# Kernel optimization log

Measured on AMD Instinct MI355X. Metric: run time of the kernel, lower is better.

Reference implementation:

```python
import jax, jax.numpy as jnp
import numpy as np

N_QUBITS = 4
N_LAYERS = 2


def setup_inputs() -> dict:
    key = jax.random.key(0)
    ks = jax.random.split(key, 8)
    B, S, D, H, O = 64, 4096, 20, 64, 3
    rn = lambda k, shape: jax.random.normal(k, shape, dtype=jnp.float32)
    sc = lambda fan: np.float32(1.0 / np.sqrt(fan))
    return {
        "x": rn(ks[0], (B, S, D)),
        "W_embed": rn(ks[1], (H, D)) * sc(D),
        "b_embed": jnp.zeros((H,), jnp.float32),
        "W_c2q": rn(ks[2], (N_QUBITS, H)) * sc(H),
        "b_c2q": jnp.zeros((N_QUBITS,), jnp.float32),
        "q_weights": rn(ks[3], (N_LAYERS, N_QUBITS, 3)) * np.float32(0.1),
        "W_q2c": rn(ks[4], (H, N_QUBITS)) * sc(N_QUBITS),
        "b_q2c": jnp.zeros((H,), jnp.float32),
        "W_out": rn(ks[5], (O, H)) * sc(H),
        "b_out": jnp.zeros((O,), jnp.float32),
    }


def _rot_matrix(phi, theta, omega):
    # PennyLane Rot(phi, theta, omega) = RZ(omega) @ RY(theta) @ RZ(phi)
    c = jnp.cos(theta * 0.5)
    s = jnp.sin(theta * 0.5)
    ep = jnp.exp(-0.5j * (phi + omega))  # e^{-i(phi+omega)/2}
    em = jnp.exp(-0.5j * (phi - omega))  # e^{-i(phi-omega)/2}
    row0 = jnp.stack([ep * c, -jnp.conj(em) * s])
    row1 = jnp.stack([em * s, jnp.conj(ep) * c])
    return jnp.stack([row0, row1]).astype(jnp.complex64)  # [2,2]


def _apply_1q(state, U, q):
    # state: [N,2,2,2,2], U: [2,2] shared across the batch
    ax = 1 + q
    s = jnp.moveaxis(state, ax, -1)
    s = jnp.einsum('...a,ba->...b', s, U)
    return jnp.moveaxis(s, -1, ax)


def _cnot(state, q):
    # control qubit q (axis 1+q), target qubit q+1 (axis 2+q)
    ac = 1 + q
    s0 = jnp.take(state, 0, axis=ac)
    # after removing control axis, the target axis index becomes ac
    s1 = jnp.flip(jnp.take(state, 1, axis=ac), axis=ac)
    return jnp.stack([s0, s1], axis=ac)


def _quantum_layer(q_in, weights):
    # q_in: [N, n_qubits] angles; weights: [n_layers, n_qubits, 3]
    half = q_in * 0.5
    v = jnp.stack([jnp.cos(half), jnp.sin(half)], axis=-1).astype(jnp.complex64)  # [N,4,2]
    # RY(inputs[i]) applied to |0...0> -> product state
    state = jnp.einsum('na,nb,nc,nd->nabcd', v[:, 0], v[:, 1], v[:, 2], v[:, 3])
    for layer in range(N_LAYERS):
        for q in range(N_QUBITS):
            U = _rot_matrix(weights[layer, q, 0], weights[layer, q, 1], weights[layer, q, 2])
            state = _apply_1q(state, U, q)
        for q in range(N_QUBITS - 1):
            state = _cnot(state, q)
    probs = state.real ** 2 + state.imag ** 2  # [N,2,2,2,2]
    z = []
    for q in range(N_QUBITS):
        axes = tuple(a for a in range(1, N_QUBITS + 1) if a != 1 + q)
        p = jnp.sum(probs, axis=axes)  # [N,2]
        z.append(p[:, 0] - p[:, 1])   # <Z_q>
    return jnp.stack(z, axis=-1)  # [N, n_qubits]


def reference(x, W_embed, b_embed, W_c2q, b_c2q, q_weights, W_q2c, b_q2c, W_out, b_out):
    B, S, _ = x.shape
    h = jax.nn.relu(jnp.einsum('bsd,hd->bsh', x, W_embed) + b_embed)      # [B,S,H]
    q_in = jnp.tanh(jnp.einsum('bsh,qh->bsq', h, W_c2q) + b_c2q)          # [B,S,4]
    z = _quantum_layer(q_in.reshape(B * S, N_QUBITS), q_weights)          # [B*S,4]
    z = z.reshape(B, S, N_QUBITS)
    h2 = jnp.einsum('bsq,hq->bsh', z, W_q2c) + b_q2c                      # [B,S,H]
    coords = jnp.einsum('bsh,oh->bso', h2, W_out) + b_out                 # [B,S,3]
    return coords
```

## Files before the change

kernel.cpp:

```cpp
#include <hip/hip_runtime.h>

typedef __bf16 bf16x8 __attribute__((ext_vector_type(8)));
typedef float f32x4 __attribute__((ext_vector_type(4)));
typedef float f32x2 __attribute__((ext_vector_type(2)));

#define NQ 4
#define NLAYERS 2

#define OFF_UCOEF 0
#define OFF_WC    64
#define OFF_UR    96
#define OFF_UI    352
#define OFF_W     608
#define OFF_G     704

__device__ __forceinline__ float fast_tanh(float v) {
  const float e = __expf(2.f * v);
  return 1.f - 2.f * __builtin_amdgcn_rcpf(e + 1.f);
}

__global__ __launch_bounds__(256, 4) void fused_kernel(
    const float* __restrict__ x,
    const float* __restrict__ Wemb,
    const float* __restrict__ bemb,
    const float* __restrict__ Wc2q,
    const float* __restrict__ bc2q,
    const float* __restrict__ qw,
    const float* __restrict__ Wq2c,
    const float* __restrict__ bq2c,
    const float* __restrict__ Wout,
    const float* __restrict__ bout,
    float* __restrict__ out, int N) {
  __shared__ __attribute__((aligned(16))) float smem[4 * 2048];
  __shared__ __attribute__((aligned(16))) float Cs01[3 * 56];
  __shared__ __attribute__((aligned(16))) float Cs2[3 * 28];
  __shared__ float offsS[3];

  if ((int)(blockIdx.x << 8) >= N) return;

  const int tid = threadIdx.x;
  const int lane = tid & 63;
  const int warp = tid >> 6;
  const int wbase = (int)(blockIdx.x << 8) + (warp << 6);
  const int g = lane >> 4;
  const int cc = lane & 15;
  float* ws = &smem[warp * 2048];
  const f32x4 zero4 = {0.f, 0.f, 0.f, 0.f};

  float4 xr[5];
  {
    const float4* x4 = reinterpret_cast<const float4*>(x);
    const size_t max4 = (size_t)N * 5 - 1;
    const size_t base4 = (size_t)wbase * 5;
#pragma unroll
    for (int i = 0; i < 5; ++i) {
      size_t gi = base4 + (size_t)(i * 64 + lane);
      xr[i] = x4[gi <= max4 ? gi : max4];
    }
  }

  bf16x8 Aemb[4];
#pragma unroll
  for (int ht = 0; ht < 4; ++ht) {
    const int h = ht * 16 + cc;
    const float* wr = Wemb + h * 20;
    float t0 = 0.f, t1 = 0.f, t2 = 0.f, t3 = 0.f, t4 = 0.f, t5 = 0.f, t6 = 0.f, t7 = 0.f;
    if (g < 2) {
      const float4 v0 = *(const float4*)(wr + g * 8);
      const float4 v1 = *(const float4*)(wr + g * 8 + 4);
      t0 = v0.x; t1 = v0.y; t2 = v0.z; t3 = v0.w;
      t4 = v1.x; t5 = v1.y; t6 = v1.z; t7 = v1.w;
    } else if (g == 2) {
      const float4 v0 = *(const float4*)(wr + 16);
      t0 = v0.x; t1 = v0.y; t2 = v0.z; t3 = v0.w;
      t4 = bemb[h];
    }
    Aemb[ht][0] = (__bf16)t0; Aemb[ht][1] = (__bf16)t1;
    Aemb[ht][2] = (__bf16)t2; Aemb[ht][3] = (__bf16)t3;
    Aemb[ht][4] = (__bf16)t4; Aemb[ht][5] = (__bf16)t5;
    Aemb[ht][6] = (__bf16)t6; Aemb[ht][7] = (__bf16)t7;
  }

  bf16x8 A2[2];
#pragma unroll
  for (int t = 0; t < 2; ++t) {
#pragma unroll
    for (int j = 0; j < 8; ++j) {
      const int mu = t * 32 + ((j >> 2) << 4) + (g << 2) + (j & 3);
      A2[t][j] = (__bf16)Wc2q[(cc & 3) * 64 + mu];
    }
  }

  if (tid < 64) {
    const int gate = tid >> 3, comp = tid & 7;
    const float phi   = qw[gate * 3 + 0];
    const float theta = qw[gate * 3 + 1];
    const float omega = qw[gate * 3 + 2];
    const bool mid = (comp >= 2 && comp <= 5);
    const float cs = mid ? __sinf(0.5f * theta) : __cosf(0.5f * theta);
    const float ang = mid ? -0.5f * (phi - omega) : -0.5f * (phi + omega);
    const float tr = ((comp & 1) == 0) ? __cosf(ang) : __sinf(ang);
    const float sgn = (comp == 2 || comp == 7) ? -1.f : 1.f;
    smem[OFF_UCOEF + gate * 8 + comp] = sgn * tr * cs;
  } else if (tid < 76) {
    const int e = tid - 64, o = e >> 2, q = e & 3;
    float s = 0.f;
    for (int h = 0; h < 64; ++h) s += Wout[o * 64 + h] * Wq2c[h * 4 + q];
    smem[OFF_WC + e] = s;
  } else if (tid < 79) {
    const int o = tid - 76;
    float s = bout[o];
    for (int h = 0; h < 64; ++h) s += Wout[o * 64 + h] * bq2c[h];
    offsS[o] = s;
  }
  __syncthreads();

  {
    const int col = tid >> 4, amp = tid & 15;
    float re = (amp == col) ? 1.f : 0.f, im = 0.f;
#pragma unroll
    for (int layer = 0; layer < NLAYERS; ++layer) {
#pragma unroll
      for (int q = 0; q < NQ; ++q) {
        const int gate = layer * NQ + q;
        const int bit = 8 >> q;
        const bool lo = !(amp & bit);
        const float cr1 = smem[OFF_UCOEF + gate * 8 + (lo ? 0 : 6)];
        const float ci1 = smem[OFF_UCOEF + gate * 8 + (lo ? 1 : 7)];
        const float cr2 = smem[OFF_UCOEF + gate * 8 + (lo ? 2 : 4)];
        const float ci2 = smem[OFF_UCOEF + gate * 8 + (lo ? 3 : 5)];
        const float pr = __shfl_xor(re, bit);
        const float pi = __shfl_xor(im, bit);
        const float mr = re, mi = im;
        re = cr1 * mr - ci1 * mi + cr2 * pr - ci2 * pi;
        im = cr1 * mi + ci1 * mr + cr2 * pi + ci2 * pr;
      }
#pragma unroll
      for (int q = 0; q < NQ - 1; ++q) {
        const int cb = 8 >> q, tb = 4 >> q;
        const float pr = __shfl_xor(re, tb);
        const float pi = __shfl_xor(im, tb);
        if (amp & cb) { re = pr; im = pi; }
      }
    }
    smem[OFF_UR + amp * 16 + col] = re;
    smem[OFF_UI + amp * 16 + col] = im;
  }
  if (tid < 48) {
    const int o = tid >> 4, k = tid & 15;
    float s = 0.f;
#pragma unroll
    for (int q = 0; q < NQ; ++q) {
      const float t = smem[OFF_WC + o * 4 + q];
      s += ((k >> (3 - q)) & 1) ? -t : t;
    }
    smem[OFF_W + tid] = s;
  }
  __syncthreads();

  {
    const int i = tid >> 4, j = tid & 15;
    float s0 = 0.f, s1 = 0.f, s2 = 0.f;
#pragma unroll
    for (int k = 0; k < 16; ++k) {
      const float S = smem[OFF_UR + k * 16 + i] * smem[OFF_UR + k * 16 + j] +
                      smem[OFF_UI + k * 16 + i] * smem[OFF_UI + k * 16 + j];
      s0 = fmaf(smem[OFF_W + k], S, s0);
      s1 = fmaf(smem[OFF_W + 16 + k], S, s1);
      s2 = fmaf(smem[OFF_W + 32 + k], S, s2);
    }
    smem[OFF_G + (i * 16 + j)] = s0;
    smem[OFF_G + 256 + (i * 16 + j)] = s1;
    smem[OFF_G + 512 + (i * 16 + j)] = s2;
  }
  __syncthreads();

  if (tid < 243) {
    const int o = tid / 81, t = tid % 81;
    const int tv0 = t / 27, tv1 = (t / 9) % 3, tv2 = (t / 3) % 3, tv3 = t % 3;
    const int tv[4] = {tv0, tv1, tv2, tv3};
    int xmask = 0, zmask = 0;
#pragma unroll
    for (int q = 0; q < 4; ++q) {
      const int b = 8 >> q;
      if (tv[q] == 2) xmask |= b;
      else if (tv[q] == 1) zmask |= b;
    }
    float s = 0.f;
#pragma unroll
    for (int i = 0; i < 16; ++i) {
      const float sgn = (__popc(i & zmask) & 1) ? -1.f : 1.f;
      s += sgn * smem[OFF_G + o * 256 + i * 16 + (i ^ xmask)];
    }
    const float val = s * 0.0625f;
    if (o < 2) Cs01[tv0 * 56 + 2 * (t % 27) + o] = val;
    else Cs2[tv0 * 28 + (t % 27)] = val;
  } else if (tid < 249) {
    const int p = tid - 243;
    Cs01[(p >> 1) * 56 + 54 + (p & 1)] = 0.f;
  } else if (tid < 252) {
    Cs2[(tid - 249) * 28 + 27] = 0.f;
  }
  __syncthreads();

  {
#pragma unroll
    for (int i = 0; i < 5; ++i) {
      const int m = i * 64 + lane;
      const int el = m / 5, ch = m % 5;
      *(float4*)&ws[el * 32 + ((ch * 4) ^ ((el & 7) << 2))] = xr[i];
    }
    const float4 bias4 = {1.f, 0.f, 0.f, 0.f};
    const float4 z4 = {0.f, 0.f, 0.f, 0.f};
    const int sw = (lane & 7) << 2;
    *(float4*)&ws[lane * 32 + ((5 * 4) ^ sw)] = bias4;
    *(float4*)&ws[lane * 32 + ((6 * 4) ^ sw)] = z4;
    *(float4*)&ws[lane * 32 + ((7 * 4) ^ sw)] = z4;
  }

  f32x4 av = zero4;
#pragma unroll
  for (int rt = 0; rt < 4; ++rt) {
    const int el = rt * 16 + cc;
    const int sw = (el & 7) << 2;
    const float4 u0 = *(const float4*)&ws[el * 32 + ((g * 8 + 0) ^ sw)];
    const float4 u1 = *(const float4*)&ws[el * 32 + ((g * 8 + 4) ^ sw)];
    bf16x8 B;
    B[0] = (__bf16)u0.x; B[1] = (__bf16)u0.y; B[2] = (__bf16)u0.z; B[3] = (__bf16)u0.w;
    B[4] = (__bf16)u1.x; B[5] = (__bf16)u1.y; B[6] = (__bf16)u1.z; B[7] = (__bf16)u1.w;

    const f32x4 acc0 = __builtin_amdgcn_mfma_f32_16x16x32_bf16(Aemb[0], B, zero4, 0, 0, 0);
    const f32x4 acc1 = __builtin_amdgcn_mfma_f32_16x16x32_bf16(Aemb[1], B, zero4, 0, 0, 0);
    const f32x4 acc2 = __builtin_amdgcn_mfma_f32_16x16x32_bf16(Aemb[2], B, zero4, 0, 0, 0);
    const f32x4 acc3 = __builtin_amdgcn_mfma_f32_16x16x32_bf16(Aemb[3], B, zero4, 0, 0, 0);

    bf16x8 P0, P1;
#pragma unroll
    for (int j = 0; j < 8; ++j) {
      P0[j] = (__bf16)fmaxf(((j >> 2) ? acc1 : acc0)[j & 3], 0.f);
      P1[j] = (__bf16)fmaxf(((j >> 2) ? acc3 : acc2)[j & 3], 0.f);
    }
    f32x4 a2 = __builtin_amdgcn_mfma_f32_16x16x32_bf16(A2[0], P0, zero4, 0, 0, 0);
    a2 = __builtin_amdgcn_mfma_f32_16x16x32_bf16(A2[1], P1, a2, 0, 0, 0);

    if (g == rt) av = a2;
  }

  const float a0 = fast_tanh(av[0] + bc2q[0]);
  const float a1 = fast_tanh(av[1] + bc2q[1]);
  const float a2v = fast_tanh(av[2] + bc2q[2]);
  const float a3 = fast_tanh(av[3] + bc2q[3]);

  const float f0v[3] = {1.f, __cosf(a0), __sinf(a0)};
  const float f1v[3] = {1.f, __cosf(a1), __sinf(a1)};
  const float f2v[3] = {1.f, __cosf(a2v), __sinf(a2v)};
  const float f3v[3] = {1.f, __cosf(a3), __sinf(a3)};

  float T23[9];
#pragma unroll
  for (int i2 = 0; i2 < 3; ++i2)
#pragma unroll
    for (int i3 = 0; i3 < 3; ++i3) T23[i2 * 3 + i3] = f2v[i2] * f3v[i3];
  float T[28];
#pragma unroll
  for (int i1 = 0; i1 < 3; ++i1)
#pragma unroll
    for (int k = 0; k < 9; ++k) T[i1 * 9 + k] = f1v[i1] * T23[k];
  T[27] = 0.f;

  f32x2 y01 = {offsS[0], offsS[1]};
  float y2 = offsS[2];
#pragma unroll
  for (int i0 = 0; i0 < 3; ++i0) {
    f32x2 s01 = {0.f, 0.f};
#pragma unroll
    for (int kk = 0; kk < 14; ++kk) {
      const float4 cp = *(const float4*)&Cs01[i0 * 56 + kk * 4];
      const f32x2 lo = {cp.x, cp.y};
      const f32x2 hi = {cp.z, cp.w};
      s01 += lo * T[2 * kk];
      s01 += hi * T[2 * kk + 1];
    }
    float s2v = 0.f;
#pragma unroll
    for (int kk = 0; kk < 7; ++kk) {
      const float4 c2 = *(const float4*)&Cs2[i0 * 28 + kk * 4];
      s2v = fmaf(c2.x, T[4 * kk + 0], s2v);
      s2v = fmaf(c2.y, T[4 * kk + 1], s2v);
      s2v = fmaf(c2.z, T[4 * kk + 2], s2v);
      s2v = fmaf(c2.w, T[4 * kk + 3], s2v);
    }
    y01 += s01 * f0v[i0];
    y2 = fmaf(f0v[i0], s2v, y2);
  }

  if (wbase + 64 <= N) {
    ws[lane * 3 + 0] = y01[0];
    ws[lane * 3 + 1] = y01[1];
    ws[lane * 3 + 2] = y2;
    if (lane < 48) {
      const float4 v = *(const float4*)&ws[lane * 4];
      reinterpret_cast<float4*>(out + (size_t)wbase * 3)[lane] = v;
    }
  } else {
    const int eo = wbase + lane;
    if (eo < N) {
      out[eo * 3 + 0] = y01[0];
      out[eo * 3 + 1] = y01[1];
      out[eo * 3 + 2] = y2;
    }
  }
}

extern "C" void kernel_launch(void* const* d_in, const int* in_sizes, int n_in,
                              void* d_out, int out_size, void* d_ws, size_t ws_size,
                              hipStream_t stream) {
  const float* x    = (const float*)d_in[0];
  const float* Wemb = (const float*)d_in[1];
  const float* bemb = (const float*)d_in[2];
  const float* Wc2q = (const float*)d_in[3];
  const float* bc2q = (const float*)d_in[4];
  const float* qw   = (const float*)d_in[5];
  const float* Wq2c = (const float*)d_in[6];
  const float* bq2c = (const float*)d_in[7];
  const float* Wout = (const float*)d_in[8];
  const float* bout = (const float*)d_in[9];
  float* out = (float*)d_out;

  const int N = in_sizes[0] / 20;

  hipLaunchKernelGGL(fused_kernel, dim3((N + 255) / 256), dim3(256), 0, stream,
                     x, Wemb, bemb, Wc2q, bc2q, qw, Wq2c, bq2c, Wout, bout, out, N);
}
```

Measured before the change: 25.42 us.

## Parallelize weight folding with wave reductions and shrink x staging in LDS

The per-block folding of Wout·Wq2c and the bias offsets, previously done by a handful of threads running 64-iteration serial loops, is now spread across three waves using shuffle-xor reductions. The x tile is staged unpadded (20 floats per element, no swizzle), which cuts LDS use per wave from 2048 to 1280 floats, and the bias column is injected in registers instead of through LDS. Embedding and weight-fragment loads move after the barrier, and the output store drops the LDS-coalesced float4 path in favour of direct strided scalar stores. Risks include LDS bank conflicts from the unswizzled 20-float stride and less coalesced global writes.

```diff
diff --git a/kernel.cpp b/kernel.cpp
--- a/kernel.cpp
+++ b/kernel.cpp
@@ -31,20 +31,18 @@
     const float* __restrict__ Wout,
     const float* __restrict__ bout,
     float* __restrict__ out, int N) {
-  __shared__ __attribute__((aligned(16))) float smem[4 * 2048];
+  __shared__ __attribute__((aligned(16))) float smem[4 * 1280];
   __shared__ __attribute__((aligned(16))) float Cs01[3 * 56];
   __shared__ __attribute__((aligned(16))) float Cs2[3 * 28];
-  __shared__ float offsS[3];
-
-  if ((int)(blockIdx.x << 8) >= N) return;
+  __shared__ float offs[3];
 
   const int tid = threadIdx.x;
   const int lane = tid & 63;
   const int warp = tid >> 6;
-  const int wbase = (int)(blockIdx.x << 8) + (warp << 6);
+  const int wbase = (int)blockIdx.x * 256 + warp * 64;
   const int g = lane >> 4;
   const int cc = lane & 15;
-  float* ws = &smem[warp * 2048];
+  float* ws = &smem[warp * 1280];
   const f32x4 zero4 = {0.f, 0.f, 0.f, 0.f};
 
   float4 xr[5];
@@ -59,59 +57,38 @@
     }
   }
 
-  bf16x8 Aemb[4];
-#pragma unroll
-  for (int ht = 0; ht < 4; ++ht) {
-    const int h = ht * 16 + cc;
-    const float* wr = Wemb + h * 20;
-    float t0 = 0.f, t1 = 0.f, t2 = 0.f, t3 = 0.f, t4 = 0.f, t5 = 0.f, t6 = 0.f, t7 = 0.f;
-    if (g < 2) {
-      const float4 v0 = *(const float4*)(wr + g * 8);
-      const float4 v1 = *(const float4*)(wr + g * 8 + 4);
-      t0 = v0.x; t1 = v0.y; t2 = v0.z; t3 = v0.w;
-      t4 = v1.x; t5 = v1.y; t6 = v1.z; t7 = v1.w;
-    } else if (g == 2) {
-      const float4 v0 = *(const float4*)(wr + 16);
-      t0 = v0.x; t1 = v0.y; t2 = v0.z; t3 = v0.w;
-      t4 = bemb[h];
-    }
-    Aemb[ht][0] = (__bf16)t0; Aemb[ht][1] = (__bf16)t1;
-    Aemb[ht][2] = (__bf16)t2; Aemb[ht][3] = (__bf16)t3;
-    Aemb[ht][4] = (__bf16)t4; Aemb[ht][5] = (__bf16)t5;
-    Aemb[ht][6] = (__bf16)t6; Aemb[ht][7] = (__bf16)t7;
-  }
-
-  bf16x8 A2[2];
-#pragma unroll
-  for (int t = 0; t < 2; ++t) {
-#pragma unroll
-    for (int j = 0; j < 8; ++j) {
-      const int mu = t * 32 + ((j >> 2) << 4) + (g << 2) + (j & 3);
-      A2[t][j] = (__bf16)Wc2q[(cc & 3) * 64 + mu];
-    }
-  }
-
-  if (tid < 64) {
-    const int gate = tid >> 3, comp = tid & 7;
+  if (warp == 0) {
+    const int gate = lane >> 3, comp = lane & 7;
     const float phi   = qw[gate * 3 + 0];
     const float theta = qw[gate * 3 + 1];
     const float omega = qw[gate * 3 + 2];
     const bool mid = (comp >= 2 && comp <= 5);
-    const float cs = mid ? __sinf(0.5f * theta) : __cosf(0.5f * theta);
+    const float cs  = mid ? __sinf(0.5f * theta) : __cosf(0.5f * theta);
     const float ang = mid ? -0.5f * (phi - omega) : -0.5f * (phi + omega);
-    const float tr = ((comp & 1) == 0) ? __cosf(ang) : __sinf(ang);
+    const float tr  = ((comp & 1) == 0) ? __cosf(ang) : __sinf(ang);
     const float sgn = (comp == 2 || comp == 7) ? -1.f : 1.f;
     smem[OFF_UCOEF + gate * 8 + comp] = sgn * tr * cs;
-  } else if (tid < 76) {
-    const int e = tid - 64, o = e >> 2, q = e & 3;
-    float s = 0.f;
-    for (int h = 0; h < 64; ++h) s += Wout[o * 64 + h] * Wq2c[h * 4 + q];
-    smem[OFF_WC + e] = s;
-  } else if (tid < 79) {
-    const int o = tid - 76;
-    float s = bout[o];
-    for (int h = 0; h < 64; ++h) s += Wout[o * 64 + h] * bq2c[h];
-    offsS[o] = s;
+  } else {
+    const int o = warp - 1;
+    const float wo = Wout[o * 64 + lane];
+    float s0 = wo * Wq2c[lane * 4 + 0];
+    float s1 = wo * Wq2c[lane * 4 + 1];
+    float s2 = wo * Wq2c[lane * 4 + 2];
+    float s3 = wo * Wq2c[lane * 4 + 3];
+    float sb = wo * bq2c[lane];
+#pragma unroll
+    for (int m = 1; m < 64; m <<= 1) {
+      s0 += __shfl_xor(s0, m); s1 += __shfl_xor(s1, m);
+      s2 += __shfl_xor(s2, m); s3 += __shfl_xor(s3, m);
+      sb += __shfl_xor(sb, m);
+    }
+    if (lane == 0) {
+      smem[OFF_WC + o * 4 + 0] = s0;
+      smem[OFF_WC + o * 4 + 1] = s1;
+      smem[OFF_WC + o * 4 + 2] = s2;
+      smem[OFF_WC + o * 4 + 3] = s3;
+      offs[o] = sb + bout[o];
+    }
   }
   __syncthreads();
 
@@ -204,30 +181,62 @@
   __syncthreads();
 
   {
-#pragma unroll
-    for (int i = 0; i < 5; ++i) {
-      const int m = i * 64 + lane;
-      const int el = m / 5, ch = m % 5;
-      *(float4*)&ws[el * 32 + ((ch * 4) ^ ((el & 7) << 2))] = xr[i];
-    }
-    const float4 bias4 = {1.f, 0.f, 0.f, 0.f};
-    const float4 z4 = {0.f, 0.f, 0.f, 0.f};
-    const int sw = (lane & 7) << 2;
-    *(float4*)&ws[lane * 32 + ((5 * 4) ^ sw)] = bias4;
-    *(float4*)&ws[lane * 32 + ((6 * 4) ^ sw)] = z4;
-    *(float4*)&ws[lane * 32 + ((7 * 4) ^ sw)] = z4;
+    float4* ls4 = reinterpret_cast<float4*>(ws);
+#pragma unroll
+    for (int i = 0; i < 5; ++i) ls4[i * 64 + lane] = xr[i];
+  }
+
+  bf16x8 Aemb[4];
+#pragma unroll
+  for (int ht = 0; ht < 4; ++ht) {
+    const int h = ht * 16 + cc;
+    const float* wr = Wemb + h * 20;
+    float t0 = 0.f, t1 = 0.f, t2 = 0.f, t3 = 0.f, t4 = 0.f, t5 = 0.f, t6 = 0.f, t7 = 0.f;
+    if (g < 2) {
+      const float4 v0 = *(const float4*)(wr + g * 8);
+      const float4 v1 = *(const float4*)(wr + g * 8 + 4);
+      t0 = v0.x; t1 = v0.y; t2 = v0.z; t3 = v0.w;
+      t4 = v1.x; t5 = v1.y; t6 = v1.z; t7 = v1.w;
+    } else if (g == 2) {
+      const float4 v0 = *(const float4*)(wr + 16);
+      t0 = v0.x; t1 = v0.y; t2 = v0.z; t3 = v0.w;
+      t4 = bemb[h];
+    }
+    Aemb[ht][0] = (__bf16)t0; Aemb[ht][1] = (__bf16)t1;
+    Aemb[ht][2] = (__bf16)t2; Aemb[ht][3] = (__bf16)t3;
+    Aemb[ht][4] = (__bf16)t4; Aemb[ht][5] = (__bf16)t5;
+    Aemb[ht][6] = (__bf16)t6; Aemb[ht][7] = (__bf16)t7;
+  }
+
+  bf16x8 A2[2];
+#pragma unroll
+  for (int t = 0; t < 2; ++t) {
+#pragma unroll
+    for (int j = 0; j < 8; ++j) {
+      const int mu = t * 32 + ((j >> 2) << 4) + (g << 2) + (j & 3);
+      A2[t][j] = (__bf16)Wc2q[(cc & 3) * 64 + mu];
+    }
   }
 
   f32x4 av = zero4;
 #pragma unroll
   for (int rt = 0; rt < 4; ++rt) {
     const int el = rt * 16 + cc;
-    const int sw = (el & 7) << 2;
-    const float4 u0 = *(const float4*)&ws[el * 32 + ((g * 8 + 0) ^ sw)];
-    const float4 u1 = *(const float4*)&ws[el * 32 + ((g * 8 + 4) ^ sw)];
+    const float* ep = &ws[el * 20];
+    float t0 = 0.f, t1 = 0.f, t2 = 0.f, t3 = 0.f, t4 = 0.f, t5 = 0.f, t6 = 0.f, t7 = 0.f;
+    if (g < 2) {
+      const float4 v0 = *(const float4*)(ep + g * 8);
+      const float4 v1 = *(const float4*)(ep + g * 8 + 4);
+      t0 = v0.x; t1 = v0.y; t2 = v0.z; t3 = v0.w;
+      t4 = v1.x; t5 = v1.y; t6 = v1.z; t7 = v1.w;
+    } else if (g == 2) {
+      const float4 v0 = *(const float4*)(ep + 16);
+      t0 = v0.x; t1 = v0.y; t2 = v0.z; t3 = v0.w;
+      t4 = 1.f;
+    }
     bf16x8 B;
-    B[0] = (__bf16)u0.x; B[1] = (__bf16)u0.y; B[2] = (__bf16)u0.z; B[3] = (__bf16)u0.w;
-    B[4] = (__bf16)u1.x; B[5] = (__bf16)u1.y; B[6] = (__bf16)u1.z; B[7] = (__bf16)u1.w;
+    B[0] = (__bf16)t0; B[1] = (__bf16)t1; B[2] = (__bf16)t2; B[3] = (__bf16)t3;
+    B[4] = (__bf16)t4; B[5] = (__bf16)t5; B[6] = (__bf16)t6; B[7] = (__bf16)t7;
 
     const f32x4 acc0 = __builtin_amdgcn_mfma_f32_16x16x32_bf16(Aemb[0], B, zero4, 0, 0, 0);
     const f32x4 acc1 = __builtin_amdgcn_mfma_f32_16x16x32_bf16(Aemb[1], B, zero4, 0, 0, 0);
@@ -268,8 +277,8 @@
     for (int k = 0; k < 9; ++k) T[i1 * 9 + k] = f1v[i1] * T23[k];
   T[27] = 0.f;
 
-  f32x2 y01 = {offsS[0], offsS[1]};
-  float y2 = offsS[2];
+  f32x2 y01 = {offs[0], offs[1]};
+  float y2 = offs[2];
 #pragma unroll
   for (int i0 = 0; i0 < 3; ++i0) {
     f32x2 s01 = {0.f, 0.f};
@@ -294,21 +303,11 @@
     y2 = fmaf(f0v[i0], s2v, y2);
   }
 
-  if (wbase + 64 <= N) {
-    ws[lane * 3 + 0] = y01[0];
-    ws[lane * 3 + 1] = y01[1];
-    ws[lane * 3 + 2] = y2;
-    if (lane < 48) {
-      const float4 v = *(const float4*)&ws[lane * 4];
-      reinterpret_cast<float4*>(out + (size_t)wbase * 3)[lane] = v;
-    }
-  } else {
-    const int eo = wbase + lane;
-    if (eo < N) {
-      out[eo * 3 + 0] = y01[0];
-      out[eo * 3 + 1] = y01[1];
-      out[eo * 3 + 2] = y2;
-    }
+  const int eo = wbase + lane;
+  if (eo < N) {
+    out[eo * 3 + 0] = y01[0];
+    out[eo * 3 + 1] = y01[1];
+    out[eo * 3 + 2] = y2;
   }
 }
 
```

New measurement: 22.40 us. -11.9%, faster.
